# Kernel optimization log

Measured on AMD Instinct MI355X. Metric: run time of the kernel, lower is better.

The kernel has to match this reference:

```python
import jax, jax.numpy as jnp
import numpy as np

BN_EPS = 1e-5


def setup_inputs() -> dict:
    key = jax.random.key(0)
    ks = jax.random.split(key, 5)
    num = 65536
    x = jax.random.normal(ks[0], (num, 3, 256), dtype=jnp.float32)
    w1a = jax.random.normal(ks[1], (256, 768), dtype=jnp.float32) * (1.0 / np.sqrt(256))
    w2a = jax.random.normal(ks[2], (256, 768), dtype=jnp.float32) * (1.0 / np.sqrt(256))
    w1b = jax.random.normal(ks[3], (768, 768), dtype=jnp.float32) * (1.0 / np.sqrt(768))
    w2b = jax.random.normal(ks[4], (768, 768), dtype=jnp.float32) * (1.0 / np.sqrt(768))
    gamma = jnp.ones((768,), dtype=jnp.float32)
    beta = jnp.zeros((768,), dtype=jnp.float32)
    return {"x": x, "w1a": w1a, "w2a": w2a, "w1b": w1b, "w2b": w2b,
            "gamma": gamma, "beta": beta, "num": num}


def _sage_layer(h, w1, w2):
    # h: [num, 3, d_in]. For each hop, neighbors = mean of the other 2 hops
    # = (sum_over_hops - self) / 2. Then self @ w2 + neigh @ w1 (no activation,
    # matching the source which defines ReLU but never applies it).
    neigh = (h.sum(axis=1, keepdims=True) - h) * 0.5          # [num, 3, d_in]
    return jnp.einsum('nhd,de->nhe', h, w2) + jnp.einsum('nhd,de->nhe', neigh, w1)


def reference(x, w1a, w2a, w1b, w2b, gamma, beta, num):
    h = _sage_layer(x, w1a, w2a)      # [num, 3, 768]
    h = _sage_layer(h, w1b, w2b)      # [num, 3, 768]
    out = h[:, 0, :]                  # take hop 0 per graph item -> [num, 768]
    # BatchNorm1d(768), training mode: biased batch stats over the num axis
    mean = out.mean(axis=0)
    var = out.var(axis=0)             # ddof=0, matches torch normalization
    out = (out - mean) * jax.lax.rsqrt(var + BN_EPS) * gamma + beta
    return jax.nn.sigmoid(out)
```

## Files before the change

### kernel.cpp

```cpp
#include <hip/hip_runtime.h>
#include <cstdint>
#include <cstddef>

#define NSAMP 65536
#define KDIM  512
#define MDIM  768

typedef __attribute__((ext_vector_type(8))) _Float16 f16x8;
typedef __attribute__((ext_vector_type(4))) float f32x4;

union H2U { _Float16 h; unsigned short u; };
__device__ __forceinline__ unsigned short f2h(float f) {
  H2U v; v.h = (_Float16)f; return v.u;
}
__device__ __forceinline__ float h2f(unsigned short u) {
  H2U v; v.u = u; return (float)v.h;
}

__global__ __launch_bounds__(256) void prep_A_kernel(const float* __restrict__ x,
                                                     unsigned short* __restrict__ A) {
  int gid = blockIdx.x * 256 + threadIdx.x;
  int n  = gid >> 6;
  int cg = gid & 63;
  const float4* xr = (const float4*)(x + (size_t)n * 768);
  float4 a = xr[cg];
  float4 b = xr[64 + cg];
  float4 c = xr[128 + cg];
  ushort4 lo, hi;
  lo.x = f2h(a.x); lo.y = f2h(a.y); lo.z = f2h(a.z); lo.w = f2h(a.w);
  hi.x = f2h(a.x + b.x + c.x); hi.y = f2h(a.y + b.y + c.y);
  hi.z = f2h(a.z + b.z + c.z); hi.w = f2h(a.w + b.w + c.w);
  unsigned short* Arow = A + (size_t)n * KDIM;
  *(ushort4*)(Arow + cg * 4) = lo;
  *(ushort4*)(Arow + 256 + cg * 4) = hi;
}

__global__ __launch_bounds__(256) void prep_B_partial(const float* __restrict__ w1a,
                                                      const float* __restrict__ w2a,
                                                      const float* __restrict__ w1b,
                                                      const float* __restrict__ w2b,
                                                      float* __restrict__ temp) {
  int b = blockIdx.x;
  int jc = b & 3;
  int rem = b >> 2;
  int mc = rem % 3;
  int ic = rem / 3;
  int t = threadIdx.x;
  int m = mc * 256 + t;
  int i0 = ic * 8;
  int j0 = jc * 192;
  __shared__ __align__(16) float sC[8][192];
  __shared__ __align__(16) float s1[8][192];
  __shared__ __align__(16) float s2[8][192];
  for (int idx = t; idx < 8 * 192; idx += 256) {
    int ii = idx / 192, jj = idx % 192;
    float a1 = w1a[(size_t)(i0 + ii) * 768 + j0 + jj];
    float a2 = w2a[(size_t)(i0 + ii) * 768 + j0 + jj];
    s1[ii][jj] = a1; s2[ii][jj] = a2; sC[ii][jj] = a2 - 0.5f * a1;
  }
  __syncthreads();
  float acc1[8] = {0,0,0,0,0,0,0,0};
  float acc2[8] = {0,0,0,0,0,0,0,0};
  const float* pb1 = w1b + (size_t)j0 * 768 + m;
  const float* pb2 = w2b + (size_t)j0 * 768 + m;
  for (int jb = 0; jb < 192; jb += 4) {
    float F[4], Gp[4], Hh[4];
#pragma unroll
    for (int u = 0; u < 4; ++u) {
      float b1 = pb1[(size_t)(jb + u) * 768];
      float b2 = pb2[(size_t)(jb + u) * 768];
      F[u]  = b2 - 0.5f * b1;
      Gp[u] = 0.5f * b2 + 0.25f * b1;
      Hh[u] = 0.5f * b1;
    }
#pragma unroll
    for (int ii = 0; ii < 8; ++ii) {
      f32x4 c  = *(const f32x4*)&sC[ii][jb];
      f32x4 a1 = *(const f32x4*)&s1[ii][jb];
      f32x4 a2 = *(const f32x4*)&s2[ii][jb];
#pragma unroll
      for (int u = 0; u < 4; ++u) {
        acc1[ii] += c[u] * F[u];
        acc2[ii] += a1[u] * Gp[u] + a2[u] * Hh[u];
      }
    }
  }
  float* t1 = temp + ((size_t)jc * 768 + m) * 256 + i0;
  float* t2 = temp + ((size_t)(4 + jc) * 768 + m) * 256 + i0;
#pragma unroll
  for (int ii = 0; ii < 8; ++ii) { t1[ii] = acc1[ii]; t2[ii] = acc2[ii]; }
}

__global__ __launch_bounds__(256) void prep_B_convert(const float* __restrict__ temp,
                                                      unsigned short* __restrict__ Bt,
                                                      float* __restrict__ stats) {
  int idx = blockIdx.x * 256 + threadIdx.x;
  int i = idx & 255;
  int m = idx >> 8;
  const float* t1 = temp + (size_t)m * 256 + i;
  const float* t2 = temp + ((size_t)4 * 768 + m) * 256 + i;
  float v1 = 0.f, v2 = 0.f;
#pragma unroll
  for (int jc = 0; jc < 4; ++jc) {
    v1 += t1[(size_t)jc * 768 * 256];
    v2 += t2[(size_t)jc * 768 * 256];
  }
  Bt[(size_t)m * KDIM + i]       = f2h(v1);
  Bt[(size_t)m * KDIM + 256 + i] = f2h(v2);
  if (idx < 1536) stats[idx] = 0.f;
}

template <bool F16OUT>
__global__ __launch_bounds__(256) void gemm_kernel(const unsigned short* __restrict__ A,
                                                   const unsigned short* __restrict__ Bt,
                                                   float* __restrict__ outf,
                                                   unsigned short* __restrict__ outh,
                                                   float* __restrict__ stats) {
  __shared__ __align__(16) unsigned short As[2 * 128 * 64];
  __shared__ __align__(16) unsigned short Bs[2 * 128 * 64];

  int bid = blockIdx.x;
  int swz = (bid & 7) * 384 + (bid >> 3);
  int bm  = swz % 6;
  int bn  = swz / 6;
  int tid  = threadIdx.x;
  int wid  = tid >> 6;
  int lane = tid & 63;
  int quad = lane >> 4;
  int l15  = lane & 15;
  int wave_r = wid >> 1;
  int wave_c = wid & 1;

  size_t row0 = (size_t)bn * 128;
  int    col0 = bm * 128;

  f32x4 acc[4][4];
#pragma unroll
  for (int i = 0; i < 4; ++i)
#pragma unroll
    for (int j = 0; j < 4; ++j) acc[i][j] = (f32x4)(0.f);

  int rsub = lane >> 3;
  int ssw  = (lane & 7) ^ rsub;

  const unsigned short* gA0 = A  + (row0 + wid * 8 + rsub) * KDIM + ssw * 8;
  const unsigned short* gB0 = Bt + (size_t)(col0 + wid * 8 + rsub) * KDIM + ssw * 8;

#define STAGE(buf, kk)                                                              \
  do {                                                                              \
    _Pragma("unroll")                                                               \
    for (int i = 0; i < 4; ++i) {                                                   \
      int rl = i * 32 + wid * 8;                                                    \
      const unsigned short* gA = gA0 + (size_t)i * (32 * KDIM) + (kk);              \
      const unsigned short* gB = gB0 + (size_t)i * (32 * KDIM) + (kk);              \
      unsigned short* lA = As + (buf) * 8192 + rl * 64;                             \
      unsigned short* lB = Bs + (buf) * 8192 + rl * 64;                             \
      __builtin_amdgcn_global_load_lds(                                             \
          (const __attribute__((address_space(1))) void*)(uintptr_t)gA,             \
          (__attribute__((address_space(3))) void*)(uint32_t)(uintptr_t)lA, 16, 0, 0); \
      __builtin_amdgcn_global_load_lds(                                             \
          (const __attribute__((address_space(1))) void*)(uintptr_t)gB,             \
          (__attribute__((address_space(3))) void*)(uint32_t)(uintptr_t)lB, 16, 0, 0); \
    }                                                                               \
  } while (0)

#define COMPUTE(buf)                                                                \
  do {                                                                              \
    _Pragma("unroll")                                                               \
    for (int ks = 0; ks < 2; ++ks) {                                                \
      f16x8 a[4], b[4];                                                             \
      _Pragma("unroll")                                                             \
      for (int rb = 0; rb < 4; ++rb) {                                              \
        int r  = wave_r * 64 + rb * 16 + l15;                                       \
        int sl = (ks * 4 + quad) ^ (l15 & 7);                                       \
        a[rb] = *(const f16x8*)&As[(buf) * 8192 + r * 64 + sl * 8];                 \
      }                                                                             \
      _Pragma("unroll")                                                             \
      for (int cb = 0; cb < 4; ++cb) {                                              \
        int r  = wave_c * 64 + cb * 16 + l15;                                       \
        int sl = (ks * 4 + quad) ^ (l15 & 7);                                       \
        b[cb] = *(const f16x8*)&Bs[(buf) * 8192 + r * 64 + sl * 8];                 \
      }                                                                             \
      __builtin_amdgcn_s_setprio(1);                                               \
      _Pragma("unroll")                                                             \
      for (int rb = 0; rb < 4; ++rb)                                                \
        _Pragma("unroll")                                                           \
        for (int cb = 0; cb < 4; ++cb)                                              \
          acc[rb][cb] = __builtin_amdgcn_mfma_f32_16x16x32_f16(a[rb], b[cb],        \
                                                               acc[rb][cb], 0, 0, 0); \
      __builtin_amdgcn_s_setprio(0);                                               \
    }                                                                               \
  } while (0)

  STAGE(0, 0);
#pragma unroll
  for (int tt = 0; tt < 4; ++tt) {
    const int k0 = tt * 128;
    STAGE(1, k0 + 64);
    asm volatile("s_waitcnt vmcnt(8)" ::: "memory");
    __builtin_amdgcn_s_barrier();
    COMPUTE(0);
    __builtin_amdgcn_s_barrier();
    if (tt < 3) {
      STAGE(0, k0 + 128);
      asm volatile("s_waitcnt vmcnt(8)" ::: "memory");
    } else {
      asm volatile("s_waitcnt vmcnt(0)" ::: "memory");
    }
    __builtin_amdgcn_s_barrier();
    COMPUTE(1);
    __builtin_amdgcn_s_barrier();
  }
#undef STAGE
#undef COMPUTE

#pragma unroll
  for (int cb = 0; cb < 4; ++cb) {
    int col = col0 + wave_c * 64 + cb * 16 + l15;
    float s1 = 0.f, s2 = 0.f;
#pragma unroll
    for (int rb = 0; rb < 4; ++rb) {
      size_t rg = row0 + wave_r * 64 + rb * 16 + quad * 4;
#pragma unroll
      for (int reg = 0; reg < 4; ++reg) {
        float v = acc[rb][cb][reg];
        if (F16OUT) outh[(rg + reg) * MDIM + col] = f2h(v);
        else        outf[(rg + reg) * MDIM + col] = v;
        s1 += v;
        s2 += v * v;
      }
    }
    s1 += __shfl_xor(s1, 16); s1 += __shfl_xor(s1, 32);
    s2 += __shfl_xor(s2, 16); s2 += __shfl_xor(s2, 32);
    if (quad == 0) {
      atomicAdd(&stats[col], s1);
      atomicAdd(&stats[768 + col], s2);
    }
  }
}

__global__ void finalize_stats(const float* __restrict__ stats, const float* __restrict__ gamma,
                               const float* __restrict__ beta, float* __restrict__ ss) {
  int c = threadIdx.x;
  if (c < 768) {
    const float inv_n = 1.0f / 65536.0f;
    float mean = stats[c] * inv_n;
    float ex2  = stats[768 + c] * inv_n;
    float var  = ex2 - mean * mean;
    float scale = gamma[c] * rsqrtf(var + 1e-5f);
    ss[c]       = scale;
    ss[768 + c] = beta[c] - mean * scale;
  }
}

__global__ __launch_bounds__(256) void bn_sigmoid_h(const unsigned short* __restrict__ outpre,
                                                    const float* __restrict__ ss,
                                                    float* __restrict__ out) {
  int idx = blockIdx.x * 256 + threadIdx.x;
  int cg  = (idx % 96) * 8;
  f16x8 h = *(const f16x8*)(outpre + (size_t)idx * 8);
  float4 sc0 = *(const float4*)&ss[cg];
  float4 sc1 = *(const float4*)&ss[cg + 4];
  float4 sh0 = *(const float4*)&ss[768 + cg];
  float4 sh1 = *(const float4*)&ss[768 + cg + 4];
  float4 r0, r1;
  r0.x = 1.f / (1.f + __expf(-((float)h[0] * sc0.x + sh0.x)));
  r0.y = 1.f / (1.f + __expf(-((float)h[1] * sc0.y + sh0.y)));
  r0.z = 1.f / (1.f + __expf(-((float)h[2] * sc0.z + sh0.z)));
  r0.w = 1.f / (1.f + __expf(-((float)h[3] * sc0.w + sh0.w)));
  r1.x = 1.f / (1.f + __expf(-((float)h[4] * sc1.x + sh1.x)));
  r1.y = 1.f / (1.f + __expf(-((float)h[5] * sc1.y + sh1.y)));
  r1.z = 1.f / (1.f + __expf(-((float)h[6] * sc1.z + sh1.z)));
  r1.w = 1.f / (1.f + __expf(-((float)h[7] * sc1.w + sh1.w)));
  ((float4*)out)[(size_t)idx * 2]     = r0;
  ((float4*)out)[(size_t)idx * 2 + 1] = r1;
}

__global__ __launch_bounds__(256) void bn_sigmoid_f(float* __restrict__ out,
                                                    const float* __restrict__ ss) {
  int idx = blockIdx.x * 256 + threadIdx.x;
  int cg  = (idx % 192) * 4;
  float4 v  = ((const float4*)out)[idx];
  float4 sc = *(const float4*)&ss[cg];
  float4 sh = *(const float4*)&ss[768 + cg];
  v.x = 1.f / (1.f + __expf(-(v.x * sc.x + sh.x)));
  v.y = 1.f / (1.f + __expf(-(v.y * sc.y + sh.y)));
  v.z = 1.f / (1.f + __expf(-(v.z * sc.z + sh.z)));
  v.w = 1.f / (1.f + __expf(-(v.w * sc.w + sh.w)));
  ((float4*)out)[idx] = v;
}

extern "C" void kernel_launch(void* const* d_in, const int* in_sizes, int n_in,
                              void* d_out, int out_size, void* d_ws, size_t ws_size,
                              hipStream_t stream) {
  const float* x     = (const float*)d_in[0];
  const float* w1a   = (const float*)d_in[1];
  const float* w2a   = (const float*)d_in[2];
  const float* w1b   = (const float*)d_in[3];
  const float* w2b   = (const float*)d_in[4];
  const float* gamma = (const float*)d_in[5];
  const float* beta  = (const float*)d_in[6];
  float* out = (float*)d_out;

  size_t offA     = 0;
  size_t offBt    = offA + (size_t)NSAMP * KDIM * 2;
  size_t offTemp  = offBt + (size_t)MDIM * KDIM * 2;
  size_t offStats = offTemp + (size_t)2 * 4 * 768 * 256 * 4;
  size_t offSS    = offStats + 1536 * 4;
  size_t offOut   = (offSS + 1536 * 4 + 255) & ~(size_t)255;
  size_t needF16  = offOut + (size_t)NSAMP * MDIM * 2;

  unsigned short* A    = (unsigned short*)((char*)d_ws + offA);
  unsigned short* Bt   = (unsigned short*)((char*)d_ws + offBt);
  float* temp          = (float*)((char*)d_ws + offTemp);
  float* stats         = (float*)((char*)d_ws + offStats);
  float* ss            = (float*)((char*)d_ws + offSS);
  unsigned short* oh   = (unsigned short*)((char*)d_ws + offOut);
  bool f16stage = ws_size >= needF16;

  prep_A_kernel<<<NSAMP * 64 / 256, 256, 0, stream>>>(x, A);
  prep_B_partial<<<384, 256, 0, stream>>>(w1a, w2a, w1b, w2b, temp);
  prep_B_convert<<<768, 256, 0, stream>>>(temp, Bt, stats);
  if (f16stage) {
    gemm_kernel<true><<<(NSAMP / 128) * (MDIM / 128), 256, 0, stream>>>(A, Bt, nullptr, oh, stats);
    finalize_stats<<<1, 768, 0, stream>>>(stats, gamma, beta, ss);
    bn_sigmoid_h<<<(size_t)NSAMP * MDIM / 8 / 256, 256, 0, stream>>>(oh, ss, out);
  } else {
    gemm_kernel<false><<<(NSAMP / 128) * (MDIM / 128), 256, 0, stream>>>(A, Bt, out, nullptr, stats);
    finalize_stats<<<1, 768, 0, stream>>>(stats, gamma, beta, ss);
    bn_sigmoid_f<<<(size_t)NSAMP * MDIM / 4 / 256, 256, 0, stream>>>(out, ss);
  }
}
```

Before: 572.6 us.

## Enlarge GEMM tile to 256x256 with 8 waves and simpler double buffering

The GEMM block tile grows from 128x128 to 256x256, using 512 threads (8 waves in a 2x4 grid), each wave computing 128x64 with 32 accumulators. This halves the global and LDS reloads per output element and cuts the number of blocks to 768. The hand-tuned vmcnt-based pipeline is replaced by a plain double-buffer loop with __syncthreads. The larger LDS footprint (128KB) and higher register use lower occupancy, and the simpler synchronisation may expose load latency.

```diff
diff --git a/kernel.cpp b/kernel.cpp
--- a/kernel.cpp
+++ b/kernel.cpp
@@ -111,32 +111,32 @@
 }
 
 template <bool F16OUT>
-__global__ __launch_bounds__(256) void gemm_kernel(const unsigned short* __restrict__ A,
-                                                   const unsigned short* __restrict__ Bt,
-                                                   float* __restrict__ outf,
-                                                   unsigned short* __restrict__ outh,
-                                                   float* __restrict__ stats) {
-  __shared__ __align__(16) unsigned short As[2 * 128 * 64];
-  __shared__ __align__(16) unsigned short Bs[2 * 128 * 64];
+__global__ __launch_bounds__(512, 2) void gemm_kernel(const unsigned short* __restrict__ A,
+                                                      const unsigned short* __restrict__ Bt,
+                                                      float* __restrict__ outf,
+                                                      unsigned short* __restrict__ outh,
+                                                      float* __restrict__ stats) {
+  __shared__ __align__(16) unsigned short As[2 * 256 * 64];
+  __shared__ __align__(16) unsigned short Bs[2 * 256 * 64];
 
   int bid = blockIdx.x;
-  int swz = (bid & 7) * 384 + (bid >> 3);
-  int bm  = swz % 6;
-  int bn  = swz / 6;
+  int swz = (bid & 7) * 96 + (bid >> 3);
+  int bm  = swz % 3;
+  int bn  = swz / 3;
   int tid  = threadIdx.x;
   int wid  = tid >> 6;
   int lane = tid & 63;
   int quad = lane >> 4;
   int l15  = lane & 15;
-  int wave_r = wid >> 1;
-  int wave_c = wid & 1;
-
-  size_t row0 = (size_t)bn * 128;
-  int    col0 = bm * 128;
-
-  f32x4 acc[4][4];
-#pragma unroll
-  for (int i = 0; i < 4; ++i)
+  int wave_r = wid >> 2;
+  int wave_c = wid & 3;
+
+  size_t row0 = (size_t)bn * 256;
+  int    col0 = bm * 256;
+
+  f32x4 acc[8][4];
+#pragma unroll
+  for (int i = 0; i < 8; ++i)
 #pragma unroll
     for (int j = 0; j < 4; ++j) acc[i][j] = (f32x4)(0.f);
 
@@ -146,15 +146,15 @@
   const unsigned short* gA0 = A  + (row0 + wid * 8 + rsub) * KDIM + ssw * 8;
   const unsigned short* gB0 = Bt + (size_t)(col0 + wid * 8 + rsub) * KDIM + ssw * 8;
 
-#define STAGE(buf, kk)                                                              \
+#define STAGE(buf, kt)                                                              \
   do {                                                                              \
     _Pragma("unroll")                                                               \
     for (int i = 0; i < 4; ++i) {                                                   \
-      int rl = i * 32 + wid * 8;                                                    \
-      const unsigned short* gA = gA0 + (size_t)i * (32 * KDIM) + (kk);              \
-      const unsigned short* gB = gB0 + (size_t)i * (32 * KDIM) + (kk);              \
-      unsigned short* lA = As + (buf) * 8192 + rl * 64;                             \
-      unsigned short* lB = Bs + (buf) * 8192 + rl * 64;                             \
+      int rl = i * 64 + wid * 8;                         \
+      const unsigned short* gA = gA0 + (size_t)(i * 64) * KDIM + (kt) * 64;         \
+      const unsigned short* gB = gB0 + (size_t)(i * 64) * KDIM + (kt) * 64;         \
+      unsigned short* lA = As + (buf) * 16384 + rl * 64;           \
+      unsigned short* lB = Bs + (buf) * 16384 + rl * 64;                            \
       __builtin_amdgcn_global_load_lds(                                             \
           (const __attribute__((address_space(1))) void*)(uintptr_t)gA,             \
           (__attribute__((address_space(3))) void*)(uint32_t)(uintptr_t)lA, 16, 0, 0); \
@@ -168,22 +168,22 @@
   do {                                                                              \
     _Pragma("unroll")                                                               \
     for (int ks = 0; ks < 2; ++ks) {                                                \
-      f16x8 a[4], b[4];                                                             \
+      f16x8 a[8], b[4];                                                             \
       _Pragma("unroll")                                                             \
-      for (int rb = 0; rb < 4; ++rb) {                                              \
-        int r  = wave_r * 64 + rb * 16 + l15;                                       \
+      for (int rb = 0; rb < 8; ++rb) {                                              \
+        int r  = wave_r * 128 + rb * 16 + l15;                                      \
         int sl = (ks * 4 + quad) ^ (l15 & 7);                                       \
-        a[rb] = *(const f16x8*)&As[(buf) * 8192 + r * 64 + sl * 8];                 \
+        a[rb] = *(const f16x8*)&As[(buf) * 16384 + r * 64 + sl * 8];                \
       }                                                                             \
       _Pragma("unroll")                                                             \
       for (int cb = 0; cb < 4; ++cb) {                                              \
         int r  = wave_c * 64 + cb * 16 + l15;                                       \
         int sl = (ks * 4 + quad) ^ (l15 & 7);                                       \
-        b[cb] = *(const f16x8*)&Bs[(buf) * 8192 + r * 64 + sl * 8];                 \
+        b[cb] = *(const f16x8*)&Bs[(buf) * 16384 + r * 64 + sl * 8];                \
       }                                                                             \
       __builtin_amdgcn_s_setprio(1);                                               \
       _Pragma("unroll")                                                             \
-      for (int rb = 0; rb < 4; ++rb)                                                \
+      for (int rb = 0; rb < 8; ++rb)                                                \
         _Pragma("unroll")                                                           \
         for (int cb = 0; cb < 4; ++cb)                                              \
           acc[rb][cb] = __builtin_amdgcn_mfma_f32_16x16x32_f16(a[rb], b[cb],        \
@@ -193,23 +193,13 @@
   } while (0)
 
   STAGE(0, 0);
-#pragma unroll
-  for (int tt = 0; tt < 4; ++tt) {
-    const int k0 = tt * 128;
-    STAGE(1, k0 + 64);
-    asm volatile("s_waitcnt vmcnt(8)" ::: "memory");
-    __builtin_amdgcn_s_barrier();
-    COMPUTE(0);
-    __builtin_amdgcn_s_barrier();
-    if (tt < 3) {
-      STAGE(0, k0 + 128);
-      asm volatile("s_waitcnt vmcnt(8)" ::: "memory");
-    } else {
-      asm volatile("s_waitcnt vmcnt(0)" ::: "memory");
-    }
-    __builtin_amdgcn_s_barrier();
-    COMPUTE(1);
-    __builtin_amdgcn_s_barrier();
+  __syncthreads();
+#pragma unroll
+  for (int kt = 0; kt < 8; ++kt) {
+    const int buf = kt & 1;
+    if (kt < 7) STAGE(buf ^ 1, kt + 1);
+    COMPUTE(buf);
+    if (kt < 7) __syncthreads();
   }
 #undef STAGE
 #undef COMPUTE
@@ -219,8 +209,8 @@
     int col = col0 + wave_c * 64 + cb * 16 + l15;
     float s1 = 0.f, s2 = 0.f;
 #pragma unroll
-    for (int rb = 0; rb < 4; ++rb) {
-      size_t rg = row0 + wave_r * 64 + rb * 16 + quad * 4;
+    for (int rb = 0; rb < 8; ++rb) {
+      size_t rg = row0 + wave_r * 128 + rb * 16 + quad * 4;
 #pragma unroll
       for (int reg = 0; reg < 4; ++reg) {
         float v = acc[rb][cb][reg];
@@ -322,11 +312,11 @@
   prep_B_partial<<<384, 256, 0, stream>>>(w1a, w2a, w1b, w2b, temp);
   prep_B_convert<<<768, 256, 0, stream>>>(temp, Bt, stats);
   if (f16stage) {
-    gemm_kernel<true><<<(NSAMP / 128) * (MDIM / 128), 256, 0, stream>>>(A, Bt, nullptr, oh, stats);
+    gemm_kernel<true><<<(NSAMP / 256) * (MDIM / 256), 512, 0, stream>>>(A, Bt, nullptr, oh, stats);
     finalize_stats<<<1, 768, 0, stream>>>(stats, gamma, beta, ss);
     bn_sigmoid_h<<<(size_t)NSAMP * MDIM / 8 / 256, 256, 0, stream>>>(oh, ss, out);
   } else {
-    gemm_kernel<false><<<(NSAMP / 128) * (MDIM / 128), 256, 0, stream>>>(A, Bt, out, nullptr, stats);
+    gemm_kernel<false><<<(NSAMP / 256) * (MDIM / 256), 512, 0, stream>>>(A, Bt, out, nullptr, stats);
     finalize_stats<<<1, 768, 0, stream>>>(stats, gamma, beta, ss);
     bn_sigmoid_f<<<(size_t)NSAMP * MDIM / 4 / 256, 256, 0, stream>>>(out, ss);
   }
```

After: 570.9 us. No clear change (-0.3%).
